# Kernel tuning notes

Measured on AMD Instinct MI355X. Metric: run time of the kernel, lower is better.

Reference implementation:

```python
import jax, jax.numpy as jnp
import numpy as np

V, E, S, B, T = 100000, 64, 4, 2048, 200
D = 2 * E          # memory_vector_dim
C = E              # controller_units
CIN = 2 * E + D    # controller input: x_t (2E) + prev read (D)
P = 2 * (D + 1) + 2 * D  # (key+beta) for read & write heads + erase + add


def setup_inputs() -> dict:
    key = jax.random.key(0)
    ks = jax.random.split(key, 16)
    g = lambda k, sh, sc=0.05: jax.random.normal(k, sh, dtype=jnp.float32) * sc
    return {
        "item": jax.random.randint(ks[0], (B,), 0, V),
        "cate": jax.random.randint(ks[1], (B,), 0, V),
        "hist_item": jax.random.randint(ks[2], (B, T), 0, V),
        "hist_cate": jax.random.randint(ks[3], (B, T), 0, V),
        "mask": jnp.ones((B, T), jnp.float32),
        "embedding": g(ks[4], (V, E)),
        "gru_Wih": g(ks[5], (3 * C, CIN)),
        "gru_Whh": g(ks[6], (3 * C, C)),
        "gru_bih": jnp.zeros((3 * C,), jnp.float32),
        "gru_bhh": jnp.zeros((3 * C,), jnp.float32),
        "Wp": g(ks[7], (P, C)),
        "bp": jnp.zeros((P,), jnp.float32),
        "Wo": g(ks[8], (E, C + D)),
        "bo": jnp.zeros((E,), jnp.float32),
        "M0": g(ks[9], (S, D), 0.1),
        "fc1_w": g(ks[10], (200, 5 * E)),
        "fc1_b": jnp.zeros((200,), jnp.float32),
        "prelu1_a": jnp.full((1,), 0.25, jnp.float32),
        "fc2_w": g(ks[11], (80, 200)),
        "fc2_b": jnp.zeros((80,), jnp.float32),
        "prelu2_a": jnp.full((1,), 0.25, jnp.float32),
        "fc3_w": g(ks[12], (2, 80)),
        "fc3_b": jnp.zeros((2,), jnp.float32),
    }


def _cos_addr(k, beta, M):
    # content addressing: softmax(beta * cosine_sim(k, M))  k:[B,D] M:[B,S,D]
    kn = k / (jnp.linalg.norm(k, axis=-1, keepdims=True) + 1e-8)
    Mn = M / (jnp.linalg.norm(M, axis=-1, keepdims=True) + 1e-8)
    K = jnp.einsum('bd,bsd->bs', kn, Mn)
    return jax.nn.softmax(beta[:, None] * K, axis=-1)


def _prelu(x, a):
    return jnp.where(x > 0, x, a * x)


def _mimn_rnn(hist_emb, mask, gru_Wih, gru_Whh, gru_bih, gru_bhh, Wp, bp, Wo, bo, M0):
    Bn = hist_emb.shape[0]
    h0 = jnp.zeros((Bn, C), hist_emb.dtype)
    r0 = jnp.zeros((Bn, D), hist_emb.dtype)
    Mi = jnp.broadcast_to(M0[None], (Bn, S, D))

    def step(carry, inp):
        h, M, read = carry
        x_t, m_t = inp                      # x_t [B,2E], m_t [B]
        ctrl_in = jnp.concatenate([x_t, read], axis=-1)
        gi = ctrl_in @ gru_Wih.T + gru_bih
        gh = h @ gru_Whh.T + gru_bhh
        i_r, i_z, i_n = jnp.split(gi, 3, axis=-1)
        h_r, h_z, h_n = jnp.split(gh, 3, axis=-1)
        rg = jax.nn.sigmoid(i_r + h_r)
        zg = jax.nn.sigmoid(i_z + h_z)
        ng = jnp.tanh(i_n + rg * h_n)
        h_new = (1.0 - zg) * ng + zg * h
        # head parameters
        p = h_new @ Wp.T + bp               # [B, P]
        hp_r, hp_w = p[:, :D + 1], p[:, D + 1:2 * (D + 1)]
        erase = jax.nn.sigmoid(p[:, 2 * (D + 1):2 * (D + 1) + D])
        add = jnp.tanh(p[:, -D:])
        k_r, beta_r = jnp.tanh(hp_r[:, :D]), jax.nn.softplus(hp_r[:, D])
        k_w, beta_w = jnp.tanh(hp_w[:, :D]), jax.nn.softplus(hp_w[:, D])
        w_r = _cos_addr(k_r, beta_r, M)
        w_w = _cos_addr(k_w, beta_w, M)
        read_new = jnp.einsum('bs,bsd->bd', w_r, M)
        M_new = M * (1.0 - w_w[..., None] * erase[:, None, :]) + w_w[..., None] * add[:, None, :]
        out = jnp.concatenate([h_new, read_new], axis=-1) @ Wo.T + bo  # [B,E]
        # sequence-length masking (dynamic_rnn semantics)
        v = (m_t > 0)[:, None]
        h = jnp.where(v, h_new, h)
        read = jnp.where(v, read_new, read)
        M = jnp.where(v[..., None], M_new, M)
        out = jnp.where(v, out, jnp.zeros_like(out))
        return (h, M, read), out

    xs = (jnp.swapaxes(hist_emb, 0, 1), jnp.swapaxes(mask, 0, 1))  # [T,B,...]
    _, outs = jax.lax.scan(step, (h0, Mi, r0), xs)
    return jnp.swapaxes(outs, 0, 1)  # [B,T,E]


def reference(item, cate, hist_item, hist_cate, mask, embedding,
              gru_Wih, gru_Whh, gru_bih, gru_bhh, Wp, bp, Wo, bo, M0,
              fc1_w, fc1_b, prelu1_a, fc2_w, fc2_b, prelu2_a, fc3_w, fc3_b):
    item_emb = jnp.concatenate([embedding[item], embedding[cate]], axis=1)      # [B,2E]
    hist_emb = jnp.concatenate([embedding[hist_item], embedding[hist_cate]], axis=2)  # [B,T,2E]
    seq_len = mask.sum(1).astype(jnp.int32)
    outputs = _mimn_rnn(hist_emb, mask, gru_Wih, gru_Whh, gru_bih, gru_bhh, Wp, bp, Wo, bo, M0)
    last_out = jnp.take_along_axis(outputs, (seq_len - 1)[:, None, None], axis=1)[:, 0, :]
    hist_sum = (hist_emb * mask[..., None]).sum(1)                              # [B,2E]
    x = jnp.concatenate([item_emb, hist_sum, last_out], axis=1)                 # [B,5E]
    x = _prelu(x @ fc1_w.T + fc1_b, prelu1_a)
    x = _prelu(x @ fc2_w.T + fc2_b, prelu2_a)
    return x @ fc3_w.T + fc3_b
```

## Files before the change

### kernel.cpp

```cpp
#include <hip/hip_runtime.h>

#define VV 100000
#define BB 2048
#define TT 200
#define GG 192
#define PP 514
#define RPB 8
#define NBT 1563

typedef _Float16 half8 __attribute__((ext_vector_type(8)));
typedef float floatx4 __attribute__((ext_vector_type(4)));
#define MFMA16(a, b, c) __builtin_amdgcn_mfma_f32_16x16x32_f16((a), (b), (c), 0, 0, 0)

#define BARRIER_LDS() do { \
    __asm__ volatile("s_waitcnt lgkmcnt(0)" ::: "memory"); \
    __builtin_amdgcn_s_barrier(); } while (0)

__device__ __forceinline__ float fsigm(float x) { return 1.0f / (1.0f + __expf(-x)); }
__device__ __forceinline__ float ftanh(float x) {
    float e = __expf(2.0f * x);
    return 1.0f - 2.0f / (e + 1.0f);
}
__device__ __forceinline__ float fsoftplus(float x) {
    float e = __expf(-fabsf(x));
    return fmaxf(x, 0.0f) + __logf(1.0f + e);
}

#define DPP_ADD(x, ctrl, rmask) \
    ((x) + __int_as_float(__builtin_amdgcn_update_dpp( \
        0, __float_as_int(x), (ctrl), (rmask), 0xf, true)))
__device__ __forceinline__ float wsum64(float x) {
    x = DPP_ADD(x, 0x111, 0xf);
    x = DPP_ADD(x, 0x112, 0xf);
    x = DPP_ADD(x, 0x114, 0xf);
    x = DPP_ADD(x, 0x118, 0xf);
    x = DPP_ADD(x, 0x142, 0xa);
    x = DPP_ADD(x, 0x143, 0xc);
    return __int_as_float(__builtin_amdgcn_readlane(__float_as_int(x), 63));
}
__device__ __forceinline__ float dot4(float4 w, float4 a) {
    return w.x * a.x + w.y * a.y + w.z * a.z + w.w * a.w;
}

__global__ __launch_bounds__(256) void prep(
    const float* __restrict__ emb,
    const float* __restrict__ Wih,
    const float* __restrict__ bih,
    const int* __restrict__ hist_item, const int* __restrict__ hist_cate,
    const float* __restrict__ mask,
    float* __restrict__ GIi, float* __restrict__ GIc,
    float* __restrict__ hist_sum, int* __restrict__ seqlen)
{
    __shared__ __align__(16) _Float16 sE16[64 * 72];
    const int tid = threadIdx.x;
    const int wv = tid >> 6, lane = tid & 63;
    const int nlo = lane & 15, kg = lane >> 4;

    if (blockIdx.x < NBT) {
        const int v0 = blockIdx.x * 64;
        for (int i = tid; i < 64 * 64; i += 256) {
            int vv = i >> 6, k = i & 63;
            int gv = v0 + vv;
            sE16[vv * 72 + k] = (gv < VV) ? (_Float16)emb[(size_t)gv * 64 + k]
                                          : (_Float16)0.f;
        }
        half8 WF[6][2];
        float bias[6];
#pragma unroll
        for (int j = 0; j < 6; ++j) {
            int pid = 6 * wv + j;
            int tb = pid / 12, nt = pid % 12;
            int n = nt * 16 + nlo;
#pragma unroll
            for (int kb = 0; kb < 2; ++kb) {
                half8 f;
#pragma unroll
                for (int q = 0; q < 8; ++q)
                    f[q] = (_Float16)Wih[n * 256 + tb * 64 + kb * 32 + kg * 8 + q];
                WF[j][kb] = f;
            }
            bias[j] = tb ? 0.f : bih[n];
        }
        __syncthreads();
#pragma unroll
        for (int mt = 0; mt < 4; ++mt) {
            const int ar = (16 * mt + nlo) * 72 + 8 * kg;
            half8 a0 = *(const half8*)&sE16[ar];
            half8 a1 = *(const half8*)&sE16[ar + 32];
#pragma unroll
            for (int j = 0; j < 6; ++j) {
                floatx4 acc = {0.f, 0.f, 0.f, 0.f};
                acc = MFMA16(a0, WF[j][0], acc);
                acc = MFMA16(a1, WF[j][1], acc);
                int pid = 6 * wv + j;
                int tb = pid / 12, nt = pid % 12;
                float* dst = tb ? GIc : GIi;
                int n = nt * 16 + nlo;
#pragma unroll
                for (int q = 0; q < 4; ++q) {
                    int gv = v0 + 16 * mt + 4 * kg + q;
                    if (gv < VV) dst[(size_t)gv * GG + n] = acc[q] + bias[j];
                }
            }
        }
    } else {
        const int hb = blockIdx.x - NBT;
        const int b = hb * 2 + (wv >> 1);
        const int* hidx = (wv & 1) ? hist_cate : hist_item;
        float acc = 0.f;
        for (int t = 0; t < TT; ++t) {
            float m = mask[(size_t)b * TT + t];
            int idx = hidx[(size_t)b * TT + t];
            acc += m * emb[(size_t)idx * 64 + lane];
        }
        hist_sum[(size_t)b * 128 + (wv & 1) * 64 + lane] = acc;
        if ((wv & 1) == 0) {
            float s = 0.f;
            for (int t = lane; t < TT; t += 64) s += mask[(size_t)b * TT + t];
            s = wsum64(s);
            if (lane == 0) seqlen[b] = (int)(s + 0.5f);
        }
    }
}

__global__ __attribute__((amdgpu_flat_work_group_size(512, 512))) void mimn_rnn(
    const int* __restrict__ hist_item, const int* __restrict__ hist_cate,
    const float* __restrict__ mask,
    const float* __restrict__ Wih,
    const float* __restrict__ Whh,
    const float* __restrict__ bhh,
    const float* __restrict__ Wp,
    const float* __restrict__ bp,
    const float* __restrict__ Wo,
    const float* __restrict__ bo,
    const float* __restrict__ M0,
    const float* __restrict__ GIi, const float* __restrict__ GIc,
    const int* __restrict__ seqlen,
    float* __restrict__ last_out)
{
    __shared__ __align__(16) float sU[4160];
    __shared__ __align__(16) _Float16 act16[16 * 200];
    __shared__ __align__(16) _Float16 hn16[16 * 72];
    __shared__ float sHnF[RPB * 64];
    __shared__ float sWpT[2 * 64];
    __shared__ unsigned char sMaskB[RPB * TT];

    const int tid = threadIdx.x;
    const int b0 = blockIdx.x * RPB;
    const int wv = tid >> 6, lane = tid & 63;
    const int nlo = lane & 15, kg = lane >> 4;
    const bool hasN = wv >= 4;

    for (int i = tid; i < 16 * 200; i += 512) act16[i] = (_Float16)0.f;
    for (int i = tid; i < 16 * 72; i += 512) hn16[i] = (_Float16)0.f;
    for (int i = tid; i < RPB * 64; i += 512) sHnF[i] = 0.f;
    if (tid < 128) sWpT[tid] = Wp[512 * 64 + tid];
    for (int i = tid; i < RPB * TT; i += 512) {
        int r = i / TT, tt = i - r * TT;
        sMaskB[i] = (mask[(size_t)(b0 + r) * TT + tt] > 0.f) ? 1 : 0;
    }

    float hreg = 0.f;
    float M1[4], M2[4];
#pragma unroll
    for (int s = 0; s < 4; ++s) {
        M1[s] = M0[s * 128 + lane];
        M2[s] = M0[s * 128 + 64 + lane];
    }
    const float bhhRZ = bhh[16 * wv + nlo];
    const float bhhN  = hasN ? bhh[128 + 16 * (wv - 4) + nlo] : 0.f;
    float bpP[4];
#pragma unroll
    for (int i = 0; i < 4; ++i) bpP[i] = bp[16 * (wv + 8 * i) + nlo];
    const float bpT = (tid < 16) ? bp[512 + (tid >> 3)] : 0.f;

    half8 WG[6];
    {
        int n = 16 * wv + nlo;
#pragma unroll
        for (int kb = 0; kb < 6; ++kb) {
            half8 f;
#pragma unroll
            for (int j = 0; j < 8; ++j) {
                int k = 32 * kb + 8 * kg + j;
                float w = (k < 128) ? Wih[n * 256 + 128 + k] : Whh[n * 64 + (k - 128)];
                f[j] = (_Float16)w;
            }
            WG[kb] = f;
        }
    }
    half8 WN[6];
    if (hasN) {
        int n = 128 + 16 * (wv - 4) + nlo;
#pragma unroll
        for (int kb = 0; kb < 4; ++kb) {
            half8 f;
#pragma unroll
            for (int j = 0; j < 8; ++j) f[j] = (_Float16)Wih[n * 256 + 128 + 32 * kb + 8 * kg + j];
            WN[kb] = f;
        }
#pragma unroll
        for (int kb = 0; kb < 2; ++kb) {
            half8 f;
#pragma unroll
            for (int j = 0; j < 8; ++j) f[j] = (_Float16)Whh[n * 64 + 32 * kb + 8 * kg + j];
            WN[4 + kb] = f;
        }
    } else {
#pragma unroll
        for (int q = 0; q < 6; ++q) WN[q] = half8{};
    }
    half8 WP[8];
#pragma unroll
    for (int i = 0; i < 4; ++i) {
        int n = 16 * (wv + 8 * i) + nlo;
#pragma unroll
        for (int kb = 0; kb < 2; ++kb) {
            half8 f;
#pragma unroll
            for (int j = 0; j < 8; ++j) f[j] = (_Float16)Wp[n * 64 + 32 * kb + 8 * kg + j];
            WP[2 * i + kb] = f;
        }
    }

    int ts = seqlen[b0 + wv] - 1;
    ts = ts < 0 ? 0 : (ts > TT - 1 ? TT - 1 : ts);

    float giA, giB, giC, gcA, gcB, gcC;
    {
        int ri = hist_item[(size_t)(b0 + wv) * TT];
        int rc = hist_cate[(size_t)(b0 + wv) * TT];
        giA = GIi[(size_t)ri * GG + lane];
        giB = GIi[(size_t)ri * GG + 64 + lane];
        giC = GIi[(size_t)ri * GG + 128 + lane];
        gcA = GIc[(size_t)rc * GG + lane];
        gcB = GIc[(size_t)rc * GG + 64 + lane];
        gcC = GIc[(size_t)rc * GG + 128 + lane];
    }
    float pKw1 = 0.f, pKw2 = 0.f, pBw = 0.f, pEr1 = 0.f, pEr2 = 0.f;
    float pAd1 = 0.f, pAd2 = 0.f;
    float nMs[4] = {1.f, 1.f, 1.f, 1.f};
    bool vldPrev = false;
    __syncthreads();

    for (int t = 0; t < TT; ++t) {
        {
            const int abase = nlo * 200 + 8 * kg;
            floatx4 accRZ = {0.f, 0.f, 0.f, 0.f};
            floatx4 accI = {0.f, 0.f, 0.f, 0.f};
            floatx4 accH = {0.f, 0.f, 0.f, 0.f};
            half8 a0 = *(const half8*)&act16[abase];
            half8 a1 = *(const half8*)&act16[abase + 32];
            half8 a2 = *(const half8*)&act16[abase + 64];
            accRZ = MFMA16(a0, WG[0], accRZ);
            accRZ = MFMA16(a1, WG[1], accRZ);
            accRZ = MFMA16(a2, WG[2], accRZ);
            if (hasN) {
                accI = MFMA16(a0, WN[0], accI);
                accI = MFMA16(a1, WN[1], accI);
                accI = MFMA16(a2, WN[2], accI);
            }
            a0 = *(const half8*)&act16[abase + 96];
            a1 = *(const half8*)&act16[abase + 128];
            a2 = *(const half8*)&act16[abase + 160];
            accRZ = MFMA16(a0, WG[3], accRZ);
            accRZ = MFMA16(a1, WG[4], accRZ);
            accRZ = MFMA16(a2, WG[5], accRZ);
            if (hasN) {
                accI = MFMA16(a0, WN[3], accI);
                accH = MFMA16(a1, WN[4], accH);
                accH = MFMA16(a2, WN[5], accH);
            }
            if (t > 0) {
                float kw1 = ftanh(pKw1), kw2 = ftanh(pKw2);
                float beta_w = fsoftplus(pBw);
                float nkw = sqrtf(wsum64(kw1 * kw1 + kw2 * kw2)) + 1e-8f;
                float Kw[4];
#pragma unroll
                for (int s = 0; s < 4; ++s) {
                    float dw = wsum64(kw1 * M1[s] + kw2 * M2[s]);
                    Kw[s] = dw / (nkw * nMs[s]);
                }
                float ww_[4];
                float mx = fmaxf(fmaxf(beta_w * Kw[0], beta_w * Kw[1]),
                                 fmaxf(beta_w * Kw[2], beta_w * Kw[3]));
                float sum = 0.f;
#pragma unroll
                for (int s = 0; s < 4; ++s) { ww_[s] = __expf(beta_w * Kw[s] - mx); sum += ww_[s]; }
                float inv = 1.f / sum;
                if (vldPrev) {
                    float er1 = fsigm(pEr1), er2 = fsigm(pEr2);
                    float ad1 = ftanh(pAd1), ad2 = ftanh(pAd2);
#pragma unroll
                    for (int s = 0; s < 4; ++s) {
                        float w = ww_[s] * inv;
                        M1[s] = M1[s] * (1.f - w * er1) + w * ad1;
                        M2[s] = M2[s] * (1.f - w * er2) + w * ad2;
                    }
                }
            }
            if (kg < 2) {
                int n = 16 * wv + nlo;
#pragma unroll
                for (int q = 0; q < 4; ++q) sU[(4 * kg + q) * 132 + n] = accRZ[q] + bhhRZ;
                if (hasN) {
                    int n64 = 16 * (wv - 4) + nlo;
#pragma unroll
                    for (int q = 0; q < 4; ++q) {
                        sU[1056 + (4 * kg + q) * 68 + n64] = accI[q];
                        sU[1600 + (4 * kg + q) * 68 + n64] = accH[q] + bhhN;
                    }
                }
            }
        }
        BARRIER_LDS();
        bool vld;
        {
            const int r = wv;
            float g_r = sU[r * 132 + lane] + giA + gcA;
            float g_z = sU[r * 132 + 64 + lane] + giB + gcB;
            float i_n = sU[1056 + r * 68 + lane] + giC + gcC;
            float h_n = sU[1600 + r * 68 + lane];
            float rg = fsigm(g_r);
            float zg = fsigm(g_z);
            float ng = ftanh(i_n + rg * h_n);
            float hn = (1.f - zg) * ng + zg * hreg;
            vld = sMaskB[r * TT + t] != 0;
            float hc = vld ? hn : hreg;
            hreg = hc;
            act16[r * 200 + 128 + lane] = (_Float16)hc;
            hn16[r * 72 + lane] = (_Float16)hn;
            sHnF[r * 64 + lane] = hn;
        }
        {
            int tn = (t + 1 < TT) ? t + 1 : TT - 1;
            int ri = hist_item[(size_t)(b0 + wv) * TT + tn];
            int rc = hist_cate[(size_t)(b0 + wv) * TT + tn];
            giA = GIi[(size_t)ri * GG + lane];
            giB = GIi[(size_t)ri * GG + 64 + lane];
            giC = GIi[(size_t)ri * GG + 128 + lane];
            gcA = GIc[(size_t)rc * GG + lane];
            gcB = GIc[(size_t)rc * GG + 64 + lane];
            gcC = GIc[(size_t)rc * GG + 128 + lane];
        }
        BARRIER_LDS();
        {
            const int bbase = nlo * 72 + 8 * kg;
            half8 b0f = *(const half8*)&hn16[bbase];
            half8 b1f = *(const half8*)&hn16[bbase + 32];
#pragma unroll
            for (int i = 0; i < 4; ++i) {
                floatx4 acc = {0.f, 0.f, 0.f, 0.f};
                acc = MFMA16(b0f, WP[2 * i], acc);
                acc = MFMA16(b1f, WP[2 * i + 1], acc);
                if (kg < 2) {
                    int n = 16 * (wv + 8 * i) + nlo;
#pragma unroll
                    for (int q = 0; q < 4; ++q) sU[(4 * kg + q) * 520 + n] = acc[q] + bpP[i];
                }
            }
        }
        if (tid < 16) {
            int r = tid & 7, j = tid >> 3;
            float acc = 0.f;
#pragma unroll
            for (int k = 0; k < 64; ++k) acc += sHnF[r * 64 + k] * sWpT[j * 64 + k];
            sU[r * 520 + 512 + j] = acc + bpT;
        }
        BARRIER_LDS();
        {
            const int row = wv;
            const int pb = row * 520;
#define PV(n) (sU[pb + (n)])
            float kr1 = ftanh(PV(lane)),       kr2 = ftanh(PV(64 + lane));
            float beta_r = fsoftplus(PV(128));
            pKw1 = PV(129 + lane); pKw2 = PV(193 + lane);
            pBw  = PV(257);
            pEr1 = PV(258 + lane); pEr2 = PV(322 + lane);
            pAd1 = PV(386 + lane); pAd2 = PV(450 + lane);
#undef PV
            float nkr = sqrtf(wsum64(kr1 * kr1 + kr2 * kr2)) + 1e-8f;
            float Kr[4];
#pragma unroll
            for (int s = 0; s < 4; ++s) {
                nMs[s] = sqrtf(wsum64(M1[s] * M1[s] + M2[s] * M2[s])) + 1e-8f;
                float dr = wsum64(kr1 * M1[s] + kr2 * M2[s]);
                Kr[s] = dr / (nkr * nMs[s]);
            }
            float wr_[4];
            {
                float mx = fmaxf(fmaxf(beta_r * Kr[0], beta_r * Kr[1]),
                                 fmaxf(beta_r * Kr[2], beta_r * Kr[3]));
                float sum = 0.f;
#pragma unroll
                for (int s = 0; s < 4; ++s) { wr_[s] = __expf(beta_r * Kr[s] - mx); sum += wr_[s]; }
                float inv = 1.f / sum;
#pragma unroll
                for (int s = 0; s < 4; ++s) wr_[s] *= inv;
            }
            float rn1 = 0.f, rn2 = 0.f;
#pragma unroll
            for (int s = 0; s < 4; ++s) { rn1 += wr_[s] * M1[s]; rn2 += wr_[s] * M2[s]; }
            vldPrev = vld;
            if (vld) {
                act16[row * 200 + lane]      = (_Float16)rn1;
                act16[row * 200 + 64 + lane] = (_Float16)rn2;
            }
            if (t == ts) {
                float* stash = &sU[pb];
                stash[lane] = rn1; stash[64 + lane] = rn2;
                __asm__ volatile("s_waitcnt lgkmcnt(0)" ::: "memory");
                float acc = bo[lane];
                const float* wo = Wo + lane * GG;
                for (int k = 0; k < 64; ++k)  acc += sHnF[row * 64 + k] * wo[k];
                for (int k = 0; k < 128; ++k) acc += stash[k] * wo[64 + k];
                if (!vld) acc = 0.f;
                last_out[(size_t)(b0 + row) * 64 + lane] = acc;
            }
        }
        BARRIER_LDS();
    }
}

__global__ __launch_bounds__(128) void final_mlp(
    const int* __restrict__ item, const int* __restrict__ cate,
    const float* __restrict__ emb,
    const float* __restrict__ hist_sum, const float* __restrict__ last_out,
    const float* __restrict__ fc1w, const float* __restrict__ fc1b,
    const float* __restrict__ pa1,
    const float* __restrict__ fc2w, const float* __restrict__ fc2b,
    const float* __restrict__ pa2,
    const float* __restrict__ fc3w, const float* __restrict__ fc3b,
    float* __restrict__ out)
{
    __shared__ float sX[320], sH1[200], sH2[80];
    int b = blockIdx.x, tid = threadIdx.x;
    int it = item[b], ct = cate[b];
    for (int i = tid; i < 320; i += 128) {
        float val;
        if (i < 64)       val = emb[(size_t)it * 64 + i];
        else if (i < 128) val = emb[(size_t)ct * 64 + (i - 64)];
        else if (i < 256) val = hist_sum[(size_t)b * 128 + (i - 128)];
        else              val = last_out[(size_t)b * 64 + (i - 256)];
        sX[i] = val;
    }
    __syncthreads();
    float a1 = pa1[0];
    for (int o = tid; o < 200; o += 128) {
        const float4* w = (const float4*)(fc1w + o * 320);
        float acc = fc1b[o];
#pragma unroll
        for (int q = 0; q < 80; ++q) acc += dot4(w[q], *(const float4*)&sX[q * 4]);
        sH1[o] = acc > 0.f ? acc : a1 * acc;
    }
    __syncthreads();
    float a2 = pa2[0];
    for (int o = tid; o < 80; o += 128) {
        const float4* w = (const float4*)(fc2w + o * 200);
        float acc = fc2b[o];
#pragma unroll
        for (int q = 0; q < 50; ++q) acc += dot4(w[q], *(const float4*)&sH1[q * 4]);
        sH2[o] = acc > 0.f ? acc : a2 * acc;
    }
    __syncthreads();
    if (tid < 2) {
        const float4* w = (const float4*)(fc3w + tid * 80);
        float acc = fc3b[tid];
#pragma unroll
        for (int q = 0; q < 20; ++q) acc += dot4(w[q], *(const float4*)&sH2[q * 4]);
        out[b * 2 + tid] = acc;
    }
}

extern "C" void kernel_launch(void* const* d_in, const int* in_sizes, int n_in,
                              void* d_out, int out_size, void* d_ws, size_t ws_size,
                              hipStream_t stream) {
    (void)in_sizes; (void)n_in; (void)out_size; (void)ws_size;
    const int*   item      = (const int*)d_in[0];
    const int*   cate      = (const int*)d_in[1];
    const int*   hist_item = (const int*)d_in[2];
    const int*   hist_cate = (const int*)d_in[3];
    const float* mask = (const float*)d_in[4];
    const float* emb  = (const float*)d_in[5];
    const float* Wih  = (const float*)d_in[6];
    const float* Whh  = (const float*)d_in[7];
    const float* bih  = (const float*)d_in[8];
    const float* bhh  = (const float*)d_in[9];
    const float* Wp   = (const float*)d_in[10];
    const float* bp   = (const float*)d_in[11];
    const float* Wo   = (const float*)d_in[12];
    const float* bo   = (const float*)d_in[13];
    const float* M0   = (const float*)d_in[14];
    const float* fc1w = (const float*)d_in[15];
    const float* fc1b = (const float*)d_in[16];
    const float* pa1  = (const float*)d_in[17];
    const float* fc2w = (const float*)d_in[18];
    const float* fc2b = (const float*)d_in[19];
    const float* pa2  = (const float*)d_in[20];
    const float* fc3w = (const float*)d_in[21];
    const float* fc3b = (const float*)d_in[22];

    float* GIi = (float*)d_ws;
    float* GIc = GIi + (size_t)VV * GG;
    float* hist_sum = GIc + (size_t)VV * GG;
    float* last_out = hist_sum + (size_t)BB * 128;
    int* seqlen = (int*)(last_out + (size_t)BB * 64);

    prep<<<NBT + BB / 2, 256, 0, stream>>>(emb, Wih, bih, hist_item, hist_cate,
                                           mask, GIi, GIc, hist_sum, seqlen);
    mimn_rnn<<<BB / RPB, 512, 0, stream>>>(hist_item, hist_cate, mask, Wih, Whh, bhh,
                                           Wp, bp, Wo, bo, M0, GIi, GIc, seqlen, last_out);
    final_mlp<<<BB, 128, 0, stream>>>(item, cate, emb, hist_sum, last_out,
                                      fc1w, fc1b, pa1, fc2w, fc2b, pa2, fc3w, fc3b,
                                      (float*)d_out);
}
```

Before: 1.060 ms.

## Fuse history sum and final MLP into the RNN kernel

Moves the masked history-embedding sum and sequence-length computation out of the prep kernel into the RNN kernel prologue, one wave per batch row. It also fuses the final three-layer MLP into the RNN kernel's epilogue, with each wave computing its row from LDS. This removes one kernel launch and the global round-trips for hist_sum, seqlen and last_out. In exchange the RNN kernel gets a serial 200-step gather before the recurrence and per-wave MLP work with only 64 lanes, which lengthens its critical path; the gather previously ran in parallel with the embedding GEMM blocks in prep.

```diff
diff --git a/kernel.cpp b/kernel.cpp
--- a/kernel.cpp
+++ b/kernel.cpp
@@ -15,6 +15,7 @@
 #define BARRIER_LDS() do { \
     __asm__ volatile("s_waitcnt lgkmcnt(0)" ::: "memory"); \
     __builtin_amdgcn_s_barrier(); } while (0)
+#define WAIT_LDS() __asm__ volatile("s_waitcnt lgkmcnt(0)" ::: "memory")
 
 __device__ __forceinline__ float fsigm(float x) { return 1.0f / (1.0f + __expf(-x)); }
 __device__ __forceinline__ float ftanh(float x) {
@@ -46,84 +47,63 @@
     const float* __restrict__ emb,
     const float* __restrict__ Wih,
     const float* __restrict__ bih,
-    const int* __restrict__ hist_item, const int* __restrict__ hist_cate,
-    const float* __restrict__ mask,
-    float* __restrict__ GIi, float* __restrict__ GIc,
-    float* __restrict__ hist_sum, int* __restrict__ seqlen)
+    float* __restrict__ GIi, float* __restrict__ GIc)
 {
     __shared__ __align__(16) _Float16 sE16[64 * 72];
     const int tid = threadIdx.x;
     const int wv = tid >> 6, lane = tid & 63;
     const int nlo = lane & 15, kg = lane >> 4;
 
-    if (blockIdx.x < NBT) {
-        const int v0 = blockIdx.x * 64;
-        for (int i = tid; i < 64 * 64; i += 256) {
-            int vv = i >> 6, k = i & 63;
-            int gv = v0 + vv;
-            sE16[vv * 72 + k] = (gv < VV) ? (_Float16)emb[(size_t)gv * 64 + k]
-                                          : (_Float16)0.f;
-        }
-        half8 WF[6][2];
-        float bias[6];
+    const int v0 = blockIdx.x * 64;
+    for (int i = tid; i < 64 * 64; i += 256) {
+        int vv = i >> 6, k = i & 63;
+        int gv = v0 + vv;
+        sE16[vv * 72 + k] = (gv < VV) ? (_Float16)emb[(size_t)gv * 64 + k]
+                                      : (_Float16)0.f;
+    }
+    half8 WF[6][2];
+    float bias[6];
+#pragma unroll
+    for (int j = 0; j < 6; ++j) {
+        int pid = 6 * wv + j;
+        int tb = pid / 12, nt = pid % 12;
+        int n = nt * 16 + nlo;
+#pragma unroll
+        for (int kb = 0; kb < 2; ++kb) {
+            half8 f;
+#pragma unroll
+            for (int q = 0; q < 8; ++q)
+                f[q] = (_Float16)Wih[n * 256 + tb * 64 + kb * 32 + kg * 8 + q];
+            WF[j][kb] = f;
+        }
+        bias[j] = tb ? 0.f : bih[n];
+    }
+    __syncthreads();
+#pragma unroll
+    for (int mt = 0; mt < 4; ++mt) {
+        const int ar = (16 * mt + nlo) * 72 + 8 * kg;
+        half8 a0 = *(const half8*)&sE16[ar];
+        half8 a1 = *(const half8*)&sE16[ar + 32];
 #pragma unroll
         for (int j = 0; j < 6; ++j) {
+            floatx4 acc = {0.f, 0.f, 0.f, 0.f};
+            acc = MFMA16(a0, WF[j][0], acc);
+            acc = MFMA16(a1, WF[j][1], acc);
             int pid = 6 * wv + j;
             int tb = pid / 12, nt = pid % 12;
+            float* dst = tb ? GIc : GIi;
             int n = nt * 16 + nlo;
 #pragma unroll
-            for (int kb = 0; kb < 2; ++kb) {
-                half8 f;
-#pragma unroll
-                for (int q = 0; q < 8; ++q)
-                    f[q] = (_Float16)Wih[n * 256 + tb * 64 + kb * 32 + kg * 8 + q];
-                WF[j][kb] = f;
-            }
-            bias[j] = tb ? 0.f : bih[n];
-        }
-        __syncthreads();
-#pragma unroll
-        for (int mt = 0; mt < 4; ++mt) {
-            const int ar = (16 * mt + nlo) * 72 + 8 * kg;
-            half8 a0 = *(const half8*)&sE16[ar];
-            half8 a1 = *(const half8*)&sE16[ar + 32];
-#pragma unroll
-            for (int j = 0; j < 6; ++j) {
-                floatx4 acc = {0.f, 0.f, 0.f, 0.f};
-                acc = MFMA16(a0, WF[j][0], acc);
-                acc = MFMA16(a1, WF[j][1], acc);
-                int pid = 6 * wv + j;
-                int tb = pid / 12, nt = pid % 12;
-                float* dst = tb ? GIc : GIi;
-                int n = nt * 16 + nlo;
-#pragma unroll
-                for (int q = 0; q < 4; ++q) {
-                    int gv = v0 + 16 * mt + 4 * kg + q;
-                    if (gv < VV) dst[(size_t)gv * GG + n] = acc[q] + bias[j];
-                }
-            }
-        }
-    } else {
-        const int hb = blockIdx.x - NBT;
-        const int b = hb * 2 + (wv >> 1);
-        const int* hidx = (wv & 1) ? hist_cate : hist_item;
-        float acc = 0.f;
-        for (int t = 0; t < TT; ++t) {
-            float m = mask[(size_t)b * TT + t];
-            int idx = hidx[(size_t)b * TT + t];
-            acc += m * emb[(size_t)idx * 64 + lane];
-        }
-        hist_sum[(size_t)b * 128 + (wv & 1) * 64 + lane] = acc;
-        if ((wv & 1) == 0) {
-            float s = 0.f;
-            for (int t = lane; t < TT; t += 64) s += mask[(size_t)b * TT + t];
-            s = wsum64(s);
-            if (lane == 0) seqlen[b] = (int)(s + 0.5f);
+            for (int q = 0; q < 4; ++q) {
+                int gv = v0 + 16 * mt + 4 * kg + q;
+                if (gv < VV) dst[(size_t)gv * GG + n] = acc[q] + bias[j];
+            }
         }
     }
 }
 
 __global__ __attribute__((amdgpu_flat_work_group_size(512, 512))) void mimn_rnn(
+    const int* __restrict__ item, const int* __restrict__ cate,
     const int* __restrict__ hist_item, const int* __restrict__ hist_cate,
     const float* __restrict__ mask,
     const float* __restrict__ Wih,
@@ -135,14 +115,21 @@
     const float* __restrict__ bo,
     const float* __restrict__ M0,
     const float* __restrict__ GIi, const float* __restrict__ GIc,
-    const int* __restrict__ seqlen,
-    float* __restrict__ last_out)
+    const float* __restrict__ emb,
+    const float* __restrict__ fc1w, const float* __restrict__ fc1b,
+    const float* __restrict__ pa1,
+    const float* __restrict__ fc2w, const float* __restrict__ fc2b,
+    const float* __restrict__ pa2,
+    const float* __restrict__ fc3w, const float* __restrict__ fc3b,
+    float* __restrict__ out)
 {
     __shared__ __align__(16) float sU[4160];
     __shared__ __align__(16) _Float16 act16[16 * 200];
     __shared__ __align__(16) _Float16 hn16[16 * 72];
     __shared__ float sHnF[RPB * 64];
     __shared__ float sWpT[2 * 64];
+    __shared__ float sHist[RPB * 128];
+    __shared__ float sLO[RPB * 64];
     __shared__ unsigned char sMaskB[RPB * TT];
 
     const int tid = threadIdx.x;
@@ -160,6 +147,25 @@
         sMaskB[i] = (mask[(size_t)(b0 + r) * TT + tt] > 0.f) ? 1 : 0;
     }
 
+    int ts;
+    {
+        const size_t base = (size_t)(b0 + wv) * TT;
+        float accI = 0.f, accC = 0.f, msum = 0.f;
+#pragma unroll 2
+        for (int t = 0; t < TT; ++t) {
+            float m = mask[base + t];
+            int ii = hist_item[base + t];
+            int ic = hist_cate[base + t];
+            accI += m * emb[(size_t)ii * 64 + lane];
+            accC += m * emb[(size_t)ic * 64 + lane];
+            msum += m;
+        }
+        sHist[wv * 128 + lane] = accI;
+        sHist[wv * 128 + 64 + lane] = accC;
+        ts = (int)(msum + 0.5f) - 1;
+        ts = ts < 0 ? 0 : (ts > TT - 1 ? TT - 1 : ts);
+    }
+
     float hreg = 0.f;
     float M1[4], M2[4];
 #pragma unroll
@@ -222,9 +228,6 @@
             WP[2 * i + kb] = f;
         }
     }
-
-    int ts = seqlen[b0 + wv] - 1;
-    ts = ts < 0 ? 0 : (ts > TT - 1 ? TT - 1 : ts);
 
     float giA, giB, giC, gcA, gcB, gcC;
     {
@@ -409,66 +412,55 @@
             if (t == ts) {
                 float* stash = &sU[pb];
                 stash[lane] = rn1; stash[64 + lane] = rn2;
-                __asm__ volatile("s_waitcnt lgkmcnt(0)" ::: "memory");
+                WAIT_LDS();
                 float acc = bo[lane];
                 const float* wo = Wo + lane * GG;
                 for (int k = 0; k < 64; ++k)  acc += sHnF[row * 64 + k] * wo[k];
                 for (int k = 0; k < 128; ++k) acc += stash[k] * wo[64 + k];
                 if (!vld) acc = 0.f;
-                last_out[(size_t)(b0 + row) * 64 + lane] = acc;
+                sLO[row * 64 + lane] = acc;
             }
         }
         BARRIER_LDS();
     }
-}
-
-__global__ __launch_bounds__(128) void final_mlp(
-    const int* __restrict__ item, const int* __restrict__ cate,
-    const float* __restrict__ emb,
-    const float* __restrict__ hist_sum, const float* __restrict__ last_out,
-    const float* __restrict__ fc1w, const float* __restrict__ fc1b,
-    const float* __restrict__ pa1,
-    const float* __restrict__ fc2w, const float* __restrict__ fc2b,
-    const float* __restrict__ pa2,
-    const float* __restrict__ fc3w, const float* __restrict__ fc3b,
-    float* __restrict__ out)
-{
-    __shared__ float sX[320], sH1[200], sH2[80];
-    int b = blockIdx.x, tid = threadIdx.x;
-    int it = item[b], ct = cate[b];
-    for (int i = tid; i < 320; i += 128) {
-        float val;
-        if (i < 64)       val = emb[(size_t)it * 64 + i];
-        else if (i < 128) val = emb[(size_t)ct * 64 + (i - 64)];
-        else if (i < 256) val = hist_sum[(size_t)b * 128 + (i - 128)];
-        else              val = last_out[(size_t)b * 64 + (i - 256)];
-        sX[i] = val;
-    }
-    __syncthreads();
-    float a1 = pa1[0];
-    for (int o = tid; o < 200; o += 128) {
-        const float4* w = (const float4*)(fc1w + o * 320);
-        float acc = fc1b[o];
-#pragma unroll
-        for (int q = 0; q < 80; ++q) acc += dot4(w[q], *(const float4*)&sX[q * 4]);
-        sH1[o] = acc > 0.f ? acc : a1 * acc;
-    }
-    __syncthreads();
-    float a2 = pa2[0];
-    for (int o = tid; o < 80; o += 128) {
-        const float4* w = (const float4*)(fc2w + o * 200);
-        float acc = fc2b[o];
-#pragma unroll
-        for (int q = 0; q < 50; ++q) acc += dot4(w[q], *(const float4*)&sH1[q * 4]);
-        sH2[o] = acc > 0.f ? acc : a2 * acc;
-    }
-    __syncthreads();
-    if (tid < 2) {
-        const float4* w = (const float4*)(fc3w + tid * 80);
-        float acc = fc3b[tid];
-#pragma unroll
-        for (int q = 0; q < 20; ++q) acc += dot4(w[q], *(const float4*)&sH2[q * 4]);
-        out[b * 2 + tid] = acc;
+
+    {
+        const int row = wv;
+        const int b = b0 + row;
+        float* X  = &sU[row * 520];
+        float* H1 = &sU[row * 520 + 320];
+        int it = item[b], ct = cate[b];
+        X[lane]       = emb[(size_t)it * 64 + lane];
+        X[64 + lane]  = emb[(size_t)ct * 64 + lane];
+        X[128 + lane] = sHist[row * 128 + lane];
+        X[192 + lane] = sHist[row * 128 + 64 + lane];
+        X[256 + lane] = sLO[row * 64 + lane];
+        WAIT_LDS();
+        float a1 = pa1[0];
+        for (int o = lane; o < 200; o += 64) {
+            const float4* w = (const float4*)(fc1w + o * 320);
+            float acc = fc1b[o];
+#pragma unroll
+            for (int q = 0; q < 80; ++q) acc += dot4(w[q], *(const float4*)&X[q * 4]);
+            H1[o] = acc > 0.f ? acc : a1 * acc;
+        }
+        WAIT_LDS();
+        float a2 = pa2[0];
+        for (int o = lane; o < 80; o += 64) {
+            const float4* w = (const float4*)(fc2w + o * 200);
+            float acc = fc2b[o];
+#pragma unroll
+            for (int q = 0; q < 50; ++q) acc += dot4(w[q], *(const float4*)&H1[q * 4]);
+            X[o] = acc > 0.f ? acc : a2 * acc;
+        }
+        WAIT_LDS();
+        if (lane < 2) {
+            const float4* w = (const float4*)(fc3w + lane * 80);
+            float acc = fc3b[lane];
+#pragma unroll
+            for (int q = 0; q < 20; ++q) acc += dot4(w[q], *(const float4*)&X[q * 4]);
+            out[(size_t)b * 2 + lane] = acc;
+        }
     }
 }
 
@@ -502,15 +494,11 @@
 
     float* GIi = (float*)d_ws;
     float* GIc = GIi + (size_t)VV * GG;
-    float* hist_sum = GIc + (size_t)VV * GG;
-    float* last_out = hist_sum + (size_t)BB * 128;
-    int* seqlen = (int*)(last_out + (size_t)BB * 64);
-
-    prep<<<NBT + BB / 2, 256, 0, stream>>>(emb, Wih, bih, hist_item, hist_cate,
-                                           mask, GIi, GIc, hist_sum, seqlen);
-    mimn_rnn<<<BB / RPB, 512, 0, stream>>>(hist_item, hist_cate, mask, Wih, Whh, bhh,
-                                           Wp, bp, Wo, bo, M0, GIi, GIc, seqlen, last_out);
-    final_mlp<<<BB, 128, 0, stream>>>(item, cate, emb, hist_sum, last_out,
-                                      fc1w, fc1b, pa1, fc2w, fc2b, pa2, fc3w, fc3b,
-                                      (float*)d_out);
-}
+
+    prep<<<NBT, 256, 0, stream>>>(emb, Wih, bih, GIi, GIc);
+    mimn_rnn<<<BB / RPB, 512, 0, stream>>>(item, cate, hist_item, hist_cate, mask,
+                                           Wih, Whh, bhh, Wp, bp, Wo, bo, M0,
+                                           GIi, GIc, emb,
+                                           fc1w, fc1b, pa1, fc2w, fc2b, pa2,
+                                           fc3w, fc3b, (float*)d_out);
+}
```

New measurement: 1.111 ms. +4.7%, slower.
